# Optimization experiments

Measured on AMD Instinct MI355X. Metric: run time of the kernel, lower is better.

The kernel has to match this reference:

```python
import jax, jax.numpy as jnp
import numpy as np

DIM = 256
HEADS = 8
DIM_HEAD = 32
INNER = HEADS * DIM_HEAD  # 256
EPS = 1e-5


def layer_norm(x, g, b):
    mu = jnp.mean(x, axis=-1, keepdims=True)
    var = jnp.var(x, axis=-1, keepdims=True)
    return (x - mu) * jax.lax.rsqrt(var + EPS) * g + b


def setup_inputs() -> dict:
    key = jax.random.key(0)
    ks = jax.random.split(key, 8)
    b, l, gx, gy, w1, w2 = 2, 5, 6, 8, 8, 8
    B, N = b * gx * gy, l * w1 * w2  # 96, 320
    x = jax.random.normal(ks[0], (b, l, gx, gy, w1, w2, DIM), dtype=jnp.float32)
    # context is the additive attention bias: [B, N, heads*N] -> (B,h,N,N)
    context = jax.random.normal(ks[1], (B, N, HEADS * N), dtype=jnp.float32) * 0.1
    s = 1.0 / np.sqrt(DIM)
    w_q = jax.random.normal(ks[2], (DIM, INNER), dtype=jnp.float32) * s
    w_kv = jax.random.normal(ks[3], (DIM, 2 * INNER), dtype=jnp.float32) * s
    w_out = jax.random.normal(ks[4], (INNER, DIM_HEAD), dtype=jnp.float32) * (1.0 / np.sqrt(INNER))
    ln_g = jnp.ones((DIM,), dtype=jnp.float32)
    ln_b = jnp.zeros((DIM,), dtype=jnp.float32)
    return {"x": x, "context": context, "w_q": w_q, "w_kv": w_kv,
            "w_out": w_out, "ln_g": ln_g, "ln_b": ln_b}


def reference(x, context, w_q, w_kv, w_out, ln_g, ln_b):
    b, l, gx, gy, w1, w2, d = x.shape
    # 'b l x y w1 w2 d -> (b x y) (l w1 w2) d'
    xs = jnp.transpose(x, (0, 2, 3, 1, 4, 5, 6)).reshape(b * gx * gy, l * w1 * w2, d)
    B, N, D = xs.shape
    xs = layer_norm(xs, ln_g, ln_b)
    q = (xs @ w_q).reshape(B, N, HEADS, DIM_HEAD).transpose(0, 2, 1, 3)   # b h n d
    kv = xs @ w_kv
    k, v = jnp.split(kv, 2, axis=-1)
    k = k.reshape(B, N, HEADS, DIM_HEAD).transpose(0, 2, 1, 3)
    v = v.reshape(B, N, HEADS, DIM_HEAD).transpose(0, 2, 1, 3)
    # bias mode with context: dots = q k^T (unscaled, faithful to source) + bias
    dots = jnp.einsum('bhnd,bhmd->bhnm', q, k)
    bias = context.reshape(B, N, HEADS, N).transpose(0, 2, 1, 3)          # b h n m
    dots = dots + bias
    attn = jax.nn.softmax(dots, axis=-1)
    out = jnp.einsum('bhnm,bhmd->bhnd', attn, v)                          # b h n d
    # 'b h (l w1 w2) d -> b l w1 w2 (h d)'
    out = out.transpose(0, 2, 1, 3).reshape(B, l, w1, w2, INNER)
    out = out @ w_out                                                     # -> dim_head
    # '(b x y) l w1 w2 d -> b l x y w1 w2 d'
    out = out.reshape(b, gx, gy, l, w1, w2, DIM_HEAD).transpose(0, 3, 1, 2, 4, 5, 6)
    return out
```

## Files before the change

### kernel.cpp

```cpp
#include <hip/hip_runtime.h>
#include <hip/hip_bf16.h>

#define BWIN 96
#define NTOK 320
#define DIMX 256
#define HEADS 8
#define DH 32
#define INNER 256
#define CTXW 2560
#define MPAD 328
#define ROWS_T 30720

typedef __bf16 bf16x8 __attribute__((ext_vector_type(8)));
typedef __bf16 bf16x4 __attribute__((ext_vector_type(4)));
typedef float f32x4 __attribute__((ext_vector_type(4)));

__global__ __launch_bounds__(256) void k_pre(
    const float* __restrict__ wq, const float* __restrict__ wkv,
    const float* __restrict__ x, const float* __restrict__ g,
    const float* __restrict__ bt, __bf16* __restrict__ wT,
    __bf16* __restrict__ y)
{
    const int t = threadIdx.x;
    if (blockIdx.x < 768) {
        const int col = blockIdx.x;
        float v;
        if (col < 256)      v = wq[t * 256 + col];
        else if (col < 512) v = wkv[t * 512 + (col - 256)];
        else                v = wkv[t * 512 + 256 + (col - 512)];
        wT[(size_t)col * 256 + t] = (__bf16)v;
        return;
    }
    const int wave = t >> 6, lane = t & 63;
    const int row = (blockIdx.x - 768) * 4 + wave;
    const int bb = row / NTOK, n = row % NTOK;
    const int b_idx = bb / 48, x_idx = (bb % 48) >> 3, y_idx = bb & 7;
    const int l_idx = n >> 6, w1_idx = (n >> 3) & 7, w2_idx = n & 7;
    const size_t src =
        ((((((size_t)b_idx * 5 + l_idx) * 6 + x_idx) * 8 + y_idx) * 8 + w1_idx) * 8 + w2_idx) * (size_t)DIMX;

    const float4 xv = *(const float4*)(x + src + lane * 4);
    float s = xv.x + xv.y + xv.z + xv.w;
    float ss = xv.x * xv.x + xv.y * xv.y + xv.z * xv.z + xv.w * xv.w;
    #pragma unroll
    for (int o = 32; o > 0; o >>= 1) {
        s += __shfl_xor(s, o);
        ss += __shfl_xor(ss, o);
    }
    const float mu = s * (1.0f / DIMX);
    const float var = ss * (1.0f / DIMX) - mu * mu;
    const float rsig = rsqrtf(var + 1e-5f);
    const float4 g4 = *(const float4*)(g + lane * 4);
    const float4 b4 = *(const float4*)(bt + lane * 4);
    bf16x4 yo;
    yo[0] = (__bf16)((xv.x - mu) * rsig * g4.x + b4.x);
    yo[1] = (__bf16)((xv.y - mu) * rsig * g4.y + b4.y);
    yo[2] = (__bf16)((xv.z - mu) * rsig * g4.z + b4.z);
    yo[3] = (__bf16)((xv.w - mu) * rsig * g4.w + b4.w);
    *(bf16x4*)(y + (size_t)row * DIMX + lane * 4) = yo;
}

__global__ __launch_bounds__(256) void k_qkv(
    const __bf16* __restrict__ y, const __bf16* __restrict__ wT,
    __bf16* __restrict__ qhb, __bf16* __restrict__ khb, __bf16* __restrict__ vhb)
{
    __shared__ __bf16 yls[128][40];
    __shared__ __bf16 wls[128][40];
    const int t = threadIdx.x, wave = t >> 6, lane = t & 63;
    const int lr = lane & 15, lg = lane >> 4;
    const int wm = wave & 1, wn = wave >> 1;
    const int bid = blockIdx.x;
    const int l2 = (bid & 7) * 180 + (bid >> 3);
    const int rbase = (l2 / 6) * 128;
    const int cbase = (l2 % 6) * 128;

    f32x4 acc[4][4];
    #pragma unroll
    for (int im = 0; im < 4; ++im)
        #pragma unroll
        for (int jn = 0; jn < 4; ++jn) acc[im][jn] = (f32x4){0.f, 0.f, 0.f, 0.f};

    const int srow = t >> 1, sseg = (t & 1) * 16;
    #pragma unroll
    for (int ks = 0; ks < 8; ++ks) {
        __syncthreads();
        #pragma unroll
        for (int j = 0; j < 2; ++j) {
            *(bf16x8*)&yls[srow][sseg + j * 8] =
                *(const bf16x8*)(y + (size_t)(rbase + srow) * DIMX + ks * 32 + sseg + j * 8);
            *(bf16x8*)&wls[srow][sseg + j * 8] =
                *(const bf16x8*)(wT + (size_t)(cbase + srow) * DIMX + ks * 32 + sseg + j * 8);
        }
        __syncthreads();

        bf16x8 yfr[4], wfr[4];
        #pragma unroll
        for (int jn = 0; jn < 4; ++jn) yfr[jn] = *(const bf16x8*)&yls[wm * 64 + jn * 16 + lr][lg * 8];
        #pragma unroll
        for (int im = 0; im < 4; ++im) wfr[im] = *(const bf16x8*)&wls[wn * 64 + im * 16 + lr][lg * 8];
        #pragma unroll
        for (int im = 0; im < 4; ++im)
            #pragma unroll
            for (int jn = 0; jn < 4; ++jn)
                acc[im][jn] = __builtin_amdgcn_mfma_f32_16x16x32_bf16(wfr[im], yfr[jn], acc[im][jn], 0, 0, 0);
    }

    #pragma unroll
    for (int im = 0; im < 4; ++im) {
        const int g = cbase + wn * 64 + im * 16 + lg * 4;
        const int which = g >> 8;
        __bf16* buf = (which == 0) ? qhb : (which == 1) ? khb : vhb;
        const int hh = (g & 255) >> 5, d = g & 31;
        #pragma unroll
        for (int jn = 0; jn < 4; ++jn) {
            const int row = rbase + wm * 64 + jn * 16 + lr;
            const int bb2 = row / NTOK, n2 = row % NTOK;
            bf16x4 p;
            #pragma unroll
            for (int i = 0; i < 4; ++i) p[i] = (__bf16)acc[im][jn][i];
            *(bf16x4*)(buf + ((size_t)(bb2 * 8 + hh) * NTOK + n2) * DH + d) = p;
        }
    }
}

__global__ __launch_bounds__(256) void k_attn(
    const __bf16* __restrict__ qhb, const __bf16* __restrict__ khb,
    const __bf16* __restrict__ vhb, const float* __restrict__ wout,
    const float* __restrict__ ctx, __bf16* __restrict__ part)
{
    __shared__ __bf16 vwls[DH][MPAD];
    __shared__ __bf16 ctxls[4][16][MPAD];
    const int t = threadIdx.x, wave = t >> 6, lane = t & 63;
    const int lr = lane & 15, lg = lane >> 4;
    const int h = blockIdx.x & 7, bb = blockIdx.x >> 3;
    const size_t panel = (size_t)(bb * 8 + h);

    {
        bf16x8 afr[2];
        #pragma unroll
        for (int rt = 0; rt < 2; ++rt)
            #pragma unroll
            for (int j = 0; j < 8; ++j)
                afr[rt][j] = (__bf16)wout[(h * 32 + lg * 8 + j) * 32 + rt * 16 + lr];
        const __bf16* vbase = vhb + panel * NTOK * DH + lg * 8;
        #pragma unroll
        for (int mt = 0; mt < 5; ++mt) {
            const int m = wave * 80 + mt * 16 + lr;
            const bf16x8 bfr = *(const bf16x8*)(vbase + (size_t)m * DH);
            #pragma unroll
            for (int rt = 0; rt < 2; ++rt) {
                const f32x4 d4 = __builtin_amdgcn_mfma_f32_16x16x32_bf16(
                    afr[rt], bfr, (f32x4){0.f, 0.f, 0.f, 0.f}, 0, 0, 0);
                #pragma unroll
                for (int i = 0; i < 4; ++i)
                    vwls[rt * 16 + lg * 4 + i][wave * 80 + mt * 16 + lr] = (__bf16)d4[i];
            }
        }
    }
    __syncthreads();

    const float* cpan = ctx + (size_t)bb * NTOK * CTXW + h * NTOK;
    const __bf16* qpan = qhb + panel * NTOK * DH;
    const __bf16* kpan = khb + panel * NTOK * DH;
    __bf16* ppan = part + ((size_t)h * ROWS_T + (size_t)bb * NTOK) * DH;

    float4 creg[20];
    {
        const float* cb = cpan + (size_t)(wave * 16) * CTXW;
        #pragma unroll
        for (int j = 0; j < 20; ++j) {
            const int f = j * 64 + lane, r = f / 80, c = f % 80;
            creg[j] = *(const float4*)(cb + (size_t)r * CTXW + c * 4);
        }
    }

    for (int it = 0; it < 5; ++it) {
        const int nw = (it * 4 + wave) * 16;

        #pragma unroll
        for (int j = 0; j < 20; ++j) {
            const int f = j * 64 + lane, r = f / 80, c = f % 80;
            bf16x4 b;
            b[0] = (__bf16)creg[j].x; b[1] = (__bf16)creg[j].y;
            b[2] = (__bf16)creg[j].z; b[3] = (__bf16)creg[j].w;
            *(bf16x4*)&ctxls[wave][r][c * 4] = b;
        }
        if (it < 4) {
            const float* cb = cpan + (size_t)((it * 4 + 4 + wave) * 16) * CTXW;
            #pragma unroll
            for (int j = 0; j < 20; ++j) {
                const int f = j * 64 + lane, r = f / 80, c = f % 80;
                creg[j] = *(const float4*)(cb + (size_t)r * CTXW + c * 4);
            }
        }

        const bf16x8 qfrag = *(const bf16x8*)(qpan + (size_t)(nw + lr) * DH + lg * 8);

        f32x4 s[20];
        #pragma unroll
        for (int mt = 0; mt < 20; ++mt) {
            const bf16x8 kfrag = *(const bf16x8*)(kpan + (size_t)(mt * 16 + lr) * DH + lg * 8);
            s[mt] = __builtin_amdgcn_mfma_f32_16x16x32_bf16(kfrag, qfrag,
                                                            (f32x4){0.f, 0.f, 0.f, 0.f}, 0, 0, 0);
        }

        #pragma unroll
        for (int mt = 0; mt < 20; ++mt) {
            const bf16x4 c4 = *(const bf16x4*)&ctxls[wave][lr][mt * 16 + lg * 4];
            #pragma unroll
            for (int i = 0; i < 4; ++i) s[mt][i] += (float)c4[i];
        }

        float mx = -3e38f;
        #pragma unroll
        for (int mt = 0; mt < 20; ++mt)
            #pragma unroll
            for (int i = 0; i < 4; ++i) mx = fmaxf(mx, s[mt][i]);
        mx = fmaxf(mx, __shfl_xor(mx, 16));
        mx = fmaxf(mx, __shfl_xor(mx, 32));

        float sum = 0.f;
        #pragma unroll
        for (int mt = 0; mt < 20; ++mt) {
            bf16x4 p4;
            #pragma unroll
            for (int i = 0; i < 4; ++i) {
                const float e = __expf(s[mt][i] - mx);
                sum += e;
                p4[i] = (__bf16)e;
            }
            *(bf16x4*)&ctxls[wave][lr][mt * 16 + lg * 4] = p4;
        }
        sum += __shfl_xor(sum, 16);
        sum += __shfl_xor(sum, 32);
        const float rinv = 1.0f / sum;

        f32x4 o0 = {0.f, 0.f, 0.f, 0.f}, o1 = {0.f, 0.f, 0.f, 0.f};
        #pragma unroll
        for (int ks = 0; ks < 10; ++ks) {
            const bf16x8 pfrag = *(const bf16x8*)&ctxls[wave][lr][ks * 32 + lg * 8];
            const bf16x8 vf0 = *(const bf16x8*)&vwls[lr][ks * 32 + lg * 8];
            const bf16x8 vf1 = *(const bf16x8*)&vwls[16 + lr][ks * 32 + lg * 8];
            o0 = __builtin_amdgcn_mfma_f32_16x16x32_bf16(vf0, pfrag, o0, 0, 0, 0);
            o1 = __builtin_amdgcn_mfma_f32_16x16x32_bf16(vf1, pfrag, o1, 0, 0, 0);
        }

        __bf16* pdst = ppan + (size_t)(nw + lr) * DH + lg * 4;
        bf16x4 r0, r1;
        #pragma unroll
        for (int i = 0; i < 4; ++i) {
            r0[i] = (__bf16)(o0[i] * rinv);
            r1[i] = (__bf16)(o1[i] * rinv);
        }
        *(bf16x4*)(pdst)      = r0;
        *(bf16x4*)(pdst + 16) = r1;
    }
}

__global__ __launch_bounds__(256) void k_red(
    const __bf16* __restrict__ part, float* __restrict__ out)
{
    const int idx = blockIdx.x * 256 + threadIdx.x;
    const int row = idx >> 3, q4 = (idx & 7) * 4;
    f32x4 a = {0.f, 0.f, 0.f, 0.f};
    #pragma unroll
    for (int h = 0; h < HEADS; ++h) {
        const bf16x4 p = *(const bf16x4*)(part + ((size_t)h * ROWS_T + row) * DH + q4);
        #pragma unroll
        for (int i = 0; i < 4; ++i) a[i] += (float)p[i];
    }
    const int bb = row / NTOK, n = row % NTOK;
    const int b_idx = bb / 48, x_idx = (bb % 48) >> 3, y_idx = bb & 7;
    const int l_idx = n >> 6, w1_idx = (n >> 3) & 7, w2_idx = n & 7;
    const size_t dst =
        ((((((size_t)b_idx * 5 + l_idx) * 6 + x_idx) * 8 + y_idx) * 8 + w1_idx) * 8 + w2_idx) * (size_t)DH;
    *(f32x4*)(out + dst + q4) = a;
}

extern "C" void kernel_launch(void* const* d_in, const int* in_sizes, int n_in,
                              void* d_out, int out_size, void* d_ws, size_t ws_size,
                              hipStream_t stream) {
    const float* x    = (const float*)d_in[0];
    const float* ctx  = (const float*)d_in[1];
    const float* wq   = (const float*)d_in[2];
    const float* wkv  = (const float*)d_in[3];
    const float* wout = (const float*)d_in[4];
    const float* ln_g = (const float*)d_in[5];
    const float* ln_b = (const float*)d_in[6];
    float* out = (float*)d_out;

    const size_t SEG = (size_t)BWIN * NTOK * INNER;
    __bf16* qhb = (__bf16*)d_ws;
    __bf16* khb = qhb + SEG;
    __bf16* vhb = khb + SEG;
    __bf16* yb  = vhb + SEG;
    __bf16* wT  = yb + SEG;
    __bf16* part = wT + 768 * 256;

    const int ROWS = BWIN * NTOK;
    k_pre<<<768 + ROWS / 4, 256, 0, stream>>>(wq, wkv, x, ln_g, ln_b, wT, yb);
    k_qkv<<<1440, 256, 0, stream>>>(yb, wT, qhb, khb, vhb);
    k_attn<<<BWIN * HEADS, 256, 0, stream>>>(qhb, khb, vhb, wout, ctx, part);
    k_red<<<ROWS * 8 / 256, 256, 0, stream>>>(part, out);
}
```

Baseline: 143.0 us.

## Drop register prefetch of context bias and stage it in half-width LDS chunks

```diff
diff --git a/kernel.cpp b/kernel.cpp
--- a/kernel.cpp
+++ b/kernel.cpp
@@ -9,6 +9,7 @@
 #define INNER 256
 #define CTXW 2560
 #define MPAD 328
+#define HPAD 168
 #define ROWS_T 30720
 
 typedef __bf16 bf16x8 __attribute__((ext_vector_type(8)));
@@ -123,13 +124,13 @@
     }
 }
 
-__global__ __launch_bounds__(256) void k_attn(
+__global__ __launch_bounds__(256, 3) void k_attn(
     const __bf16* __restrict__ qhb, const __bf16* __restrict__ khb,
     const __bf16* __restrict__ vhb, const float* __restrict__ wout,
     const float* __restrict__ ctx, __bf16* __restrict__ part)
 {
     __shared__ __bf16 vwls[DH][MPAD];
-    __shared__ __bf16 ctxls[4][16][MPAD];
+    __shared__ __bf16 cpls[4][16][HPAD];
     const int t = threadIdx.x, wave = t >> 6, lane = t & 63;
     const int lr = lane & 15, lg = lane >> 4;
     const int h = blockIdx.x & 7, bb = blockIdx.x >> 3;
@@ -164,51 +165,35 @@
     const __bf16* kpan = khb + panel * NTOK * DH;
     __bf16* ppan = part + ((size_t)h * ROWS_T + (size_t)bb * NTOK) * DH;
 
-    float4 creg[20];
-    {
-        const float* cb = cpan + (size_t)(wave * 16) * CTXW;
-        #pragma unroll
-        for (int j = 0; j < 20; ++j) {
-            const int f = j * 64 + lane, r = f / 80, c = f % 80;
-            creg[j] = *(const float4*)(cb + (size_t)r * CTXW + c * 4);
-        }
-    }
-
     for (int it = 0; it < 5; ++it) {
         const int nw = (it * 4 + wave) * 16;
-
-        #pragma unroll
-        for (int j = 0; j < 20; ++j) {
-            const int f = j * 64 + lane, r = f / 80, c = f % 80;
-            bf16x4 b;
-            b[0] = (__bf16)creg[j].x; b[1] = (__bf16)creg[j].y;
-            b[2] = (__bf16)creg[j].z; b[3] = (__bf16)creg[j].w;
-            *(bf16x4*)&ctxls[wave][r][c * 4] = b;
-        }
-        if (it < 4) {
-            const float* cb = cpan + (size_t)((it * 4 + 4 + wave) * 16) * CTXW;
-            #pragma unroll
-            for (int j = 0; j < 20; ++j) {
-                const int f = j * 64 + lane, r = f / 80, c = f % 80;
-                creg[j] = *(const float4*)(cb + (size_t)r * CTXW + c * 4);
-            }
-        }
+        const float* cb = cpan + (size_t)nw * CTXW;
 
         const bf16x8 qfrag = *(const bf16x8*)(qpan + (size_t)(nw + lr) * DH + lg * 8);
 
         f32x4 s[20];
         #pragma unroll
-        for (int mt = 0; mt < 20; ++mt) {
-            const bf16x8 kfrag = *(const bf16x8*)(kpan + (size_t)(mt * 16 + lr) * DH + lg * 8);
-            s[mt] = __builtin_amdgcn_mfma_f32_16x16x32_bf16(kfrag, qfrag,
-                                                            (f32x4){0.f, 0.f, 0.f, 0.f}, 0, 0, 0);
-        }
-
-        #pragma unroll
-        for (int mt = 0; mt < 20; ++mt) {
-            const bf16x4 c4 = *(const bf16x4*)&ctxls[wave][lr][mt * 16 + lg * 4];
-            #pragma unroll
-            for (int i = 0; i < 4; ++i) s[mt][i] += (float)c4[i];
+        for (int half = 0; half < 2; ++half) {
+            #pragma unroll
+            for (int j = 0; j < 10; ++j) {
+                const int f = j * 64 + lane, r = f / 40, c = f % 40;
+                const float4 v = *(const float4*)(cb + (size_t)r * CTXW + half * 160 + c * 4);
+                bf16x4 b;
+                b[0] = (__bf16)v.x; b[1] = (__bf16)v.y;
+                b[2] = (__bf16)v.z; b[3] = (__bf16)v.w;
+                *(bf16x4*)&cpls[wave][r][c * 4] = b;
+            }
+            #pragma unroll
+            for (int mt2 = 0; mt2 < 10; ++mt2) {
+                const int mt = half * 10 + mt2;
+                const bf16x8 kfrag = *(const bf16x8*)(kpan + (size_t)(mt * 16 + lr) * DH + lg * 8);
+                f32x4 a = __builtin_amdgcn_mfma_f32_16x16x32_bf16(kfrag, qfrag,
+                                                                  (f32x4){0.f, 0.f, 0.f, 0.f}, 0, 0, 0);
+                const bf16x4 c4 = *(const bf16x4*)&cpls[wave][lr][mt2 * 16 + lg * 4];
+                #pragma unroll
+                for (int i = 0; i < 4; ++i) a[i] += (float)c4[i];
+                s[mt] = a;
+            }
         }
 
         float mx = -3e38f;
@@ -220,30 +205,34 @@
         mx = fmaxf(mx, __shfl_xor(mx, 32));
 
         float sum = 0.f;
-        #pragma unroll
-        for (int mt = 0; mt < 20; ++mt) {
-            bf16x4 p4;
-            #pragma unroll
-            for (int i = 0; i < 4; ++i) {
-                const float e = __expf(s[mt][i] - mx);
-                sum += e;
-                p4[i] = (__bf16)e;
-            }
-            *(bf16x4*)&ctxls[wave][lr][mt * 16 + lg * 4] = p4;
+        f32x4 o0 = {0.f, 0.f, 0.f, 0.f}, o1 = {0.f, 0.f, 0.f, 0.f};
+        #pragma unroll
+        for (int half = 0; half < 2; ++half) {
+            #pragma unroll
+            for (int mt2 = 0; mt2 < 10; ++mt2) {
+                const int mt = half * 10 + mt2;
+                bf16x4 p4;
+                #pragma unroll
+                for (int i = 0; i < 4; ++i) {
+                    const float e = __expf(s[mt][i] - mx);
+                    sum += e;
+                    p4[i] = (__bf16)e;
+                }
+                *(bf16x4*)&cpls[wave][lr][mt2 * 16 + lg * 4] = p4;
+            }
+            #pragma unroll
+            for (int ks2 = 0; ks2 < 5; ++ks2) {
+                const int ks = half * 5 + ks2;
+                const bf16x8 pfrag = *(const bf16x8*)&cpls[wave][lr][ks2 * 32 + lg * 8];
+                const bf16x8 vf0 = *(const bf16x8*)&vwls[lr][ks * 32 + lg * 8];
+                const bf16x8 vf1 = *(const bf16x8*)&vwls[16 + lr][ks * 32 + lg * 8];
+                o0 = __builtin_amdgcn_mfma_f32_16x16x32_bf16(vf0, pfrag, o0, 0, 0, 0);
+                o1 = __builtin_amdgcn_mfma_f32_16x16x32_bf16(vf1, pfrag, o1, 0, 0, 0);
+            }
         }
         sum += __shfl_xor(sum, 16);
         sum += __shfl_xor(sum, 32);
         const float rinv = 1.0f / sum;
-
-        f32x4 o0 = {0.f, 0.f, 0.f, 0.f}, o1 = {0.f, 0.f, 0.f, 0.f};
-        #pragma unroll
-        for (int ks = 0; ks < 10; ++ks) {
-            const bf16x8 pfrag = *(const bf16x8*)&ctxls[wave][lr][ks * 32 + lg * 8];
-            const bf16x8 vf0 = *(const bf16x8*)&vwls[lr][ks * 32 + lg * 8];
-            const bf16x8 vf1 = *(const bf16x8*)&vwls[16 + lr][ks * 32 + lg * 8];
-            o0 = __builtin_amdgcn_mfma_f32_16x16x32_bf16(vf0, pfrag, o0, 0, 0, 0);
-            o1 = __builtin_amdgcn_mfma_f32_16x16x32_bf16(vf1, pfrag, o1, 0, 0, 0);
-        }
 
         __bf16* pdst = ppan + (size_t)(nw + lr) * DH + lg * 4;
         bf16x4 r0, r1;
```

Result: slower. 219.2 us (+53.4%).
